# Optimization experiments

Hardware: AMD Instinct MI355X
Metric: run time of the kernel (lower is better)

Reference implementation:

```python
import jax, jax.numpy as jnp
import numpy as np

B, NQ, NK = 4, 2048, 2048
DQ = DK = DV = 256
H = 8
HD = DV // H
EPS = 1e-5


def _ln(x, g, b):
    m = jnp.mean(x, axis=-1, keepdims=True)
    v = jnp.mean(jnp.square(x - m), axis=-1, keepdims=True)
    return (x - m) * jax.lax.rsqrt(v + EPS) * g + b


def setup_inputs() -> dict:
    key = jax.random.key(0)
    ks = jax.random.split(key, 12)
    s = 0.02
    return {
        "Q": jax.random.normal(ks[0], (B, NQ, DQ), jnp.float32),
        "K": jax.random.normal(ks[1], (B, NK, DK), jnp.float32),
        "Wq": jax.random.normal(ks[2], (DV, DQ), jnp.float32) * s,
        "bq": jnp.zeros((DV,), jnp.float32),
        "Wk": jax.random.normal(ks[3], (DV, DK), jnp.float32) * s,
        "bk": jnp.zeros((DV,), jnp.float32),
        "Wv": jax.random.normal(ks[4], (DV, DK), jnp.float32) * s,
        "bv": jnp.zeros((DV,), jnp.float32),
        "Wo": jax.random.normal(ks[5], (DV, DV), jnp.float32) * s,
        "bo": jnp.zeros((DV,), jnp.float32),
        "g0": jnp.ones((DV,), jnp.float32),
        "b0": jnp.zeros((DV,), jnp.float32),
        "g1": jnp.ones((DV,), jnp.float32),
        "b1": jnp.zeros((DV,), jnp.float32),
    }


def reference(Q, K, Wq, bq, Wk, bk, Wv, bv, Wo, bo, g0, b0, g1, b1):
    Qp = Q @ Wq.T + bq            # [B,NQ,DV]
    Kp = K @ Wk.T + bk            # [B,NK,DV]
    Vp = K @ Wv.T + bv            # [B,NK,DV]
    # split(head_dim, dim=2) + cat(dim=0) == reshape heads from contiguous channel chunks
    qh = Qp.reshape(B, NQ, H, HD)
    kh = Kp.reshape(B, NK, H, HD)
    vh = Vp.reshape(B, NK, H, HD)
    scores = jnp.einsum("bqhd,bkhd->bhqk", qh, kh) / jnp.sqrt(jnp.float32(HD))
    attn = jax.nn.softmax(scores, axis=-1)          # [B,H,NQ,NK]
    o = jnp.einsum("bhqk,bkhd->bqhd", attn, vh).reshape(B, NQ, DV)
    o = _ln(o, g0, b0)
    out = o + jax.nn.relu(o @ Wo.T + bo)
    out = _ln(out, g1, b1)
    return out
```

## Files before the change

### kernel.cpp

```cpp
#include <hip/hip_runtime.h>
#include <hip/hip_bf16.h>
#include <math.h>

#define DV 256
#define NH 8
#define NB 4
#define NQ 2048
#define NKK 2048

typedef __attribute__((ext_vector_type(8))) short s8v;
typedef __attribute__((ext_vector_type(16))) float fx16;

typedef const __attribute__((address_space(1))) char g1c;
typedef __attribute__((address_space(3))) char l3c;

__device__ __forceinline__ void gl_lds16(const void* g, void* l) {
    __builtin_amdgcn_global_load_lds((g1c*)g, (l3c*)l, 16, 0, 0);
}
__device__ __forceinline__ unsigned cvtpk_bf16(float lo, float hi) {
    unsigned r;
    asm("v_cvt_pk_bf16_f32 %0, %1, %2" : "=v"(r) : "v"(lo), "v"(hi));
    return r;
}
__device__ __forceinline__ ushort f2bf(float x) {
    unsigned u = __builtin_bit_cast(unsigned, x);
    return (ushort)((u + 0x7fffu + ((u >> 16) & 1u)) >> 16);
}
__device__ __forceinline__ float bf2f(ushort h) {
    return __builtin_bit_cast(float, (unsigned)h << 16);
}

__global__ __launch_bounds__(256) void prep_k(
    const float* __restrict__ Q, const float* __restrict__ K,
    const float* __restrict__ Wq, const float* __restrict__ Wk,
    const float* __restrict__ Wv, const float* __restrict__ Wo,
    ushort* __restrict__ Qc, ushort* __restrict__ Kc, ushort* __restrict__ Wf)
{
    const int i = blockIdx.x * 256 + threadIdx.x;
    const float* src;
    ushort* dst;
    if (i < 262144) {
        src = Q + (size_t)i * 8;  dst = Qc + (size_t)i * 8;
    } else if (i < 524288) {
        src = K + (size_t)(i - 262144) * 8;  dst = Kc + (size_t)(i - 262144) * 8;
    } else {
        const int j = i - 524288;
        const int w = j >> 13, c = j & 8191;
        const int bn = c >> 11, s = (c >> 8) & 7, cc = c & 255;
        const int colblk = cc >> 7, ks = (cc >> 6) & 1, g5 = (cc >> 5) & 1, l31 = cc & 31;
        const int col = bn * 64 + colblk * 32 + l31;
        const int k = s * 32 + ks * 16 + g5 * 8;
        const float* Wsrc = (w == 0) ? Wq : (w == 1) ? Wk : (w == 2) ? Wv : Wo;
        src = Wsrc + (size_t)col * 256 + k;
        dst = Wf + (size_t)j * 8;
    }
    float4 a = *(const float4*)src;
    float4 b = *(const float4*)(src + 4);
    uint4 pk;
    pk.x = cvtpk_bf16(a.x, a.y); pk.y = cvtpk_bf16(a.z, a.w);
    pk.z = cvtpk_bf16(b.x, b.y); pk.w = cvtpk_bf16(b.z, b.w);
    *(uint4*)dst = pk;
}

#define GEMM_MFMA_BODY(A_, WF_)                                                         \
    __shared__ __align__(16) char lds[2][12288];                                        \
    const int t = threadIdx.x, lane = t & 63, wv = t >> 6;                              \
    const int l31 = lane & 31, g5 = lane >> 5;                                          \
    const int bm = blockIdx.x, bn = blockIdx.y;                                         \
    const ushort* asrc0 = A_ + (size_t)(bm * 128 + (t >> 7) * 32 + (t & 31)) * 256      \
                             + ((t >> 6) & 1) * 16 + ((t >> 5) & 1) * 8;                \
    const ushort* asrc1 = asrc0 + 64 * 256;                                             \
    const ushort* wsrc  = WF_ + (size_t)(bn * 8) * 2048 + t * 8;                        \
    gl_lds16(asrc0, &lds[0][wv * 1024]);                                                \
    gl_lds16(asrc1, &lds[0][4096 + wv * 1024]);                                         \
    gl_lds16(wsrc,  &lds[0][8192 + wv * 1024]);                                         \
    __syncthreads();                                                                    \
    fx16 acc0 = {}, acc1 = {};                                                          \
    for (int s = 0; s < 8; ++s) {                                                       \
        const int buf = s & 1;                                                          \
        if (s + 1 < 8) {                                                                \
            gl_lds16(asrc0 + (s + 1) * 32, &lds[buf ^ 1][wv * 1024]);                   \
            gl_lds16(asrc1 + (s + 1) * 32, &lds[buf ^ 1][4096 + wv * 1024]);            \
            gl_lds16(wsrc + (s + 1) * 2048, &lds[buf ^ 1][8192 + wv * 1024]);           \
        }                                                                               \
        const char* Al = lds[buf];                                                      \
        const char* Wl = lds[buf] + 8192;                                               \
        s8v a0  = *(const s8v*)(Al + (wv * 2 + 0) * 1024 + lane * 16);                  \
        s8v a1  = *(const s8v*)(Al + (wv * 2 + 1) * 1024 + lane * 16);                  \
        s8v b00 = *(const s8v*)(Wl + 0 * 1024 + lane * 16);                             \
        s8v b01 = *(const s8v*)(Wl + 1 * 1024 + lane * 16);                             \
        s8v b10 = *(const s8v*)(Wl + 2 * 1024 + lane * 16);                             \
        s8v b11 = *(const s8v*)(Wl + 3 * 1024 + lane * 16);                             \
        __builtin_amdgcn_s_setprio(1);                                                  \
        acc0 = __builtin_amdgcn_mfma_f32_32x32x16_bf16(a0, b00, acc0, 0, 0, 0);         \
        acc0 = __builtin_amdgcn_mfma_f32_32x32x16_bf16(a1, b01, acc0, 0, 0, 0);         \
        acc1 = __builtin_amdgcn_mfma_f32_32x32x16_bf16(a0, b10, acc1, 0, 0, 0);         \
        acc1 = __builtin_amdgcn_mfma_f32_32x32x16_bf16(a1, b11, acc1, 0, 0, 0);         \
        __builtin_amdgcn_s_setprio(0);                                                  \
        __syncthreads();                                                                \
    }                                                                                   \
    const int row_b = bm * 128 + wv * 32;

__global__ __launch_bounds__(256) void gemm_qkv_k(
    const ushort* __restrict__ Qc, const ushort* __restrict__ Kc,
    const ushort* __restrict__ Wf,
    const float* __restrict__ bq, const float* __restrict__ bk, const float* __restrict__ bv,
    ushort* __restrict__ Qb, ushort* __restrict__ Kb, ushort* __restrict__ Vt)
{
    const int z = blockIdx.z;
    const ushort* A  = (z == 0) ? Qc : Kc;
    const ushort* WF = Wf + (size_t)z * 65536;
    const float* bias = (z == 0) ? bq : (z == 1) ? bk : bv;
    GEMM_MFMA_BODY(A, WF)
    const float CE = 0.17677669529663687f * 1.4426950408889634f;
    const float bs0 = bias[bn * 64 + l31];
    const float bs1 = bias[bn * 64 + 32 + l31];
    if (z == 0) {
#pragma unroll
        for (int r = 0; r < 16; ++r) {
            const int row_g = row_b + (r & 3) + 8 * (r >> 2) + 4 * g5;
            Qb[(size_t)row_g * 256 + bn * 64 + l31]      = f2bf((acc0[r] + bs0) * CE);
            Qb[(size_t)row_g * 256 + bn * 64 + 32 + l31] = f2bf((acc1[r] + bs1) * CE);
        }
    } else if (z == 1) {
#pragma unroll
        for (int r = 0; r < 16; ++r) {
            const int row_g = row_b + (r & 3) + 8 * (r >> 2) + 4 * g5;
            Kb[(size_t)row_g * 256 + bn * 64 + l31]      = f2bf(acc0[r] + bs0);
            Kb[(size_t)row_g * 256 + bn * 64 + 32 + l31] = f2bf(acc1[r] + bs1);
        }
    } else {
#pragma unroll
        for (int r = 0; r < 16; ++r) {
            const int row_g = row_b + (r & 3) + 8 * (r >> 2) + 4 * g5;
            const int bb = row_g >> 11, n = row_g & 2047;
            Vt[((size_t)(bb * 8 + bn * 2 + 0) * 32 + l31) * 2048 + n] = f2bf(acc0[r] + bs0);
            Vt[((size_t)(bb * 8 + bn * 2 + 1) * 32 + l31) * 2048 + n] = f2bf(acc1[r] + bs1);
        }
    }
}

__global__ __launch_bounds__(256) void flash_mfma_k(
    const ushort* __restrict__ Qb, const ushort* __restrict__ Kb,
    const ushort* __restrict__ Vt, ushort* __restrict__ Osb, float* __restrict__ L)
{
    __shared__ __align__(16) char lds[2][8192];
    const int t = threadIdx.x;
    const int lane = t & 63, wv = t >> 6;
    const int l31 = lane & 31, g5 = lane >> 5;
    const int qt = blockIdx.x, h = blockIdx.y;
    const int b = blockIdx.z >> 2, sp = blockIdx.z & 3;

    s8v qf0, qf1;
    {
        const ushort* qp = Qb + (((size_t)b * NQ + qt * 128 + wv * 32 + l31) << 8) + h * 32 + g5 * 8;
        qf0 = *(const s8v*)(qp);
        qf1 = *(const s8v*)(qp + 16);
    }
    s8v ones;
#pragma unroll
    for (int j = 0; j < 8; ++j) ones[j] = (short)0x3F80;

    const ushort* ksrc = Kb + (((size_t)b * NKK + sp * 512 + ((t >> 7) * 32 + (t & 31))) << 8)
                            + h * 32 + ((t >> 6) & 1) * 16 + ((t >> 5) & 1) * 8;
    const ushort* vsrc = Vt + (((size_t)(b * NH + h) * 32 + (t & 31)) << 11) + sp * 512
                            + (t >> 6) * 16 + ((t >> 5) & 1) * 8;

    fx16 O0 = {}, lsum = {};

    gl_lds16(ksrc, &lds[0][wv * 1024]);
    gl_lds16(vsrc, &lds[0][4096 + wv * 1024]);
    __syncthreads();

    for (int kt = 0; kt < 8; ++kt) {
        const int buf = kt & 1;
        if (kt + 1 < 8) {
            gl_lds16(ksrc + (size_t)(kt + 1) * 64 * DV, &lds[buf ^ 1][wv * 1024]);
            gl_lds16(vsrc + (kt + 1) * 64, &lds[buf ^ 1][4096 + wv * 1024]);
        }
        const char* Kl = lds[buf];
        const char* Vl = lds[buf] + 4096;
        s8v kf00 = *(const s8v*)(Kl + 0 * 1024 + lane * 16);
        s8v kf01 = *(const s8v*)(Kl + 1 * 1024 + lane * 16);
        s8v kf10 = *(const s8v*)(Kl + 2 * 1024 + lane * 16);
        s8v kf11 = *(const s8v*)(Kl + 3 * 1024 + lane * 16);
        s8v vfa[4];
        vfa[0] = *(const s8v*)(Vl + 0 * 1024 + lane * 16);
        vfa[1] = *(const s8v*)(Vl + 1 * 1024 + lane * 16);
        vfa[2] = *(const s8v*)(Vl + 2 * 1024 + lane * 16);
        vfa[3] = *(const s8v*)(Vl + 3 * 1024 + lane * 16);

        fx16 z = {};
        __builtin_amdgcn_s_setprio(1);
        fx16 Sa = __builtin_amdgcn_mfma_f32_32x32x16_bf16(kf00, qf0, z, 0, 0, 0);
        Sa = __builtin_amdgcn_mfma_f32_32x32x16_bf16(kf01, qf1, Sa, 0, 0, 0);
        fx16 Sb = __builtin_amdgcn_mfma_f32_32x32x16_bf16(kf10, qf0, z, 0, 0, 0);
        Sb = __builtin_amdgcn_mfma_f32_32x32x16_bf16(kf11, qf1, Sb, 0, 0, 0);
        __builtin_amdgcn_s_setprio(0);

        float p[32];
#pragma unroll
        for (int i = 0; i < 16; ++i) {
            p[i]      = __builtin_amdgcn_exp2f(Sa[i]);
            p[16 + i] = __builtin_amdgcn_exp2f(Sb[i]);
        }

        __builtin_amdgcn_s_setprio(1);
#pragma unroll
        for (int kt2 = 0; kt2 < 4; ++kt2) {
            const int pb = 8 * kt2;
            auto ra = __builtin_amdgcn_permlane32_swap(
                cvtpk_bf16(p[pb + 0], p[pb + 1]), cvtpk_bf16(p[pb + 4], p[pb + 5]), false, false);
            auto rb = __builtin_amdgcn_permlane32_swap(
                cvtpk_bf16(p[pb + 2], p[pb + 3]), cvtpk_bf16(p[pb + 6], p[pb + 7]), false, false);
            union { unsigned u[4]; s8v v; } pf;
            pf.u[0] = ra[0]; pf.u[1] = rb[0]; pf.u[2] = ra[1]; pf.u[3] = rb[1];
            O0   = __builtin_amdgcn_mfma_f32_32x32x16_bf16(vfa[kt2], pf.v, O0, 0, 0, 0);
            lsum = __builtin_amdgcn_mfma_f32_32x32x16_bf16(ones,    pf.v, lsum, 0, 0, 0);
        }
        __builtin_amdgcn_s_setprio(0);
        __syncthreads();
    }

    {
        const int qrow = qt * 128 + wv * 32 + l31;
        ushort* dst0 = Osb + (size_t)sp * (8192 * 256)
                     + (((size_t)b * NQ + qrow) << 8) + h * 32 + g5 * 4;
#pragma unroll
        for (int rr = 0; rr < 4; ++rr) {
            uint2 w;
            w.x = cvtpk_bf16(O0[4 * rr + 0], O0[4 * rr + 1]);
            w.y = cvtpk_bf16(O0[4 * rr + 2], O0[4 * rr + 3]);
            *(uint2*)(dst0 + 8 * rr) = w;
        }
        if (g5 == 0)
            L[(((size_t)sp * NB + b) * NH + h) * NQ + qrow] = lsum[0];
    }
}

__global__ __launch_bounds__(256) void comb_ln_k(
    const ushort* __restrict__ Osb, const float* __restrict__ L,
    const float* __restrict__ g, const float* __restrict__ bb,
    ushort* __restrict__ Yb)
{
    const int t = threadIdx.x, lane = t & 63, w = t >> 6;
    const int row = blockIdx.x * 4 + w;
    const int b = row >> 11, q = row & 2047;
    const int h = lane >> 3;
    const size_t lbase = (((size_t)b * NH + h) * NQ + q);
    const size_t LS = (size_t)NB * NH * NQ;
    const float lt = (L[lbase] + L[LS + lbase]) + (L[2 * LS + lbase] + L[3 * LS + lbase]);
    const float inv = 1.f / lt;
    const size_t SZS = (size_t)8192 * 256;
    const size_t off = (size_t)row * 256 + lane * 4;
    const ushort4 x0 = *(const ushort4*)(Osb + off);
    const ushort4 x1 = *(const ushort4*)(Osb + SZS + off);
    const ushort4 x2 = *(const ushort4*)(Osb + 2 * SZS + off);
    const ushort4 x3 = *(const ushort4*)(Osb + 3 * SZS + off);
    float4 x;
    x.x = ((bf2f(x0.x) + bf2f(x1.x)) + (bf2f(x2.x) + bf2f(x3.x))) * inv;
    x.y = ((bf2f(x0.y) + bf2f(x1.y)) + (bf2f(x2.y) + bf2f(x3.y))) * inv;
    x.z = ((bf2f(x0.z) + bf2f(x1.z)) + (bf2f(x2.z) + bf2f(x3.z))) * inv;
    x.w = ((bf2f(x0.w) + bf2f(x1.w)) + (bf2f(x2.w) + bf2f(x3.w))) * inv;
    float s  = (x.x + x.y) + (x.z + x.w);
    float sq = fmaf(x.x, x.x, fmaf(x.y, x.y, fmaf(x.z, x.z, x.w * x.w)));
    for (int off2 = 32; off2; off2 >>= 1) {
        s  += __shfl_xor(s, off2);
        sq += __shfl_xor(sq, off2);
    }
    const float mean = s * (1.f / 256.f);
    const float var  = sq * (1.f / 256.f) - mean * mean;
    const float ri   = rsqrtf(var + 1e-5f);
    const float4 gv = *(const float4*)(g + lane * 4);
    const float4 bv = *(const float4*)(bb + lane * 4);
    uint2 p;
    p.x = cvtpk_bf16((x.x - mean) * ri * gv.x + bv.x, (x.y - mean) * ri * gv.y + bv.y);
    p.y = cvtpk_bf16((x.z - mean) * ri * gv.z + bv.z, (x.w - mean) * ri * gv.w + bv.w);
    *(uint2*)(Yb + (size_t)row * 256 + lane * 4) = p;
}

__global__ __launch_bounds__(256) void gemm_ln_k(
    const ushort* __restrict__ Ain, const ushort* __restrict__ Wfo,
    const float* __restrict__ bo, const float* __restrict__ g1,
    const float* __restrict__ b1, float* __restrict__ out)
{
    __shared__ __align__(16) char alds[32768];
    __shared__ __align__(16) char wlds[2][16384];
    __shared__ float red[4][64][2];
    __shared__ float par[64][2];
    const int t = threadIdx.x, lane = t & 63, wv = t >> 6;
    const int l31 = lane & 31, g5 = lane >> 5;
    const int row0 = blockIdx.x * 64;

#pragma unroll
    for (int it = 0; it < 8; ++it) {
        const int id = it * 256 + t;
        const int s = id >> 8, rem = id & 255, kc = rem >> 6, row = rem & 63;
        gl_lds16(Ain + (size_t)(row0 + row) * 256 + s * 32 + (kc >> 1) * 16 + (kc & 1) * 8,
                 &alds[id * 16]);
    }
#pragma unroll
    for (int it = 0; it < 4; ++it) {
        const int id = it * 256 + t;
        gl_lds16(Wfo + ((size_t)(id >> 8) * 2048 + (id & 255)) * 8, &wlds[0][id * 16]);
    }
    __syncthreads();

    fx16 acc[2][2] = {};
    for (int s = 0; s < 8; ++s) {
        const int buf = s & 1;
        if (s + 1 < 8) {
#pragma unroll
            for (int it = 0; it < 4; ++it) {
                const int id = it * 256 + t;
                gl_lds16(Wfo + ((size_t)(id >> 8) * 2048 + (s + 1) * 256 + (id & 255)) * 8,
                         &wlds[buf ^ 1][id * 16]);
            }
        }
        s8v a[2][2], bf[2][2];
#pragma unroll
        for (int rb = 0; rb < 2; ++rb)
#pragma unroll
            for (int ks = 0; ks < 2; ++ks)
                a[rb][ks] = *(const s8v*)(alds + ((s * 4 + ks * 2 + g5) * 64 + rb * 32 + l31) * 16);
#pragma unroll
        for (int ks = 0; ks < 2; ++ks)
#pragma unroll
            for (int ch = 0; ch < 2; ++ch)
                bf[ks][ch] = *(const s8v*)(wlds[buf] + (wv * 256 + ch * 128 + ks * 64 + g5 * 32 + l31) * 16);
        __builtin_amdgcn_s_setprio(1);
#pragma unroll
        for (int rb = 0; rb < 2; ++rb)
#pragma unroll
            for (int ch = 0; ch < 2; ++ch) {
                acc[rb][ch] = __builtin_amdgcn_mfma_f32_32x32x16_bf16(a[rb][0], bf[0][ch], acc[rb][ch], 0, 0, 0);
                acc[rb][ch] = __builtin_amdgcn_mfma_f32_32x32x16_bf16(a[rb][1], bf[1][ch], acc[rb][ch], 0, 0, 0);
            }
        __builtin_amdgcn_s_setprio(0);
        __syncthreads();
    }

    const int cg0 = wv * 64 + l31, cg1 = cg0 + 32;
    const float bo0 = bo[cg0], bo1 = bo[cg1];
    const int s0 = cg0 >> 5, kk0 = cg0 & 31;
    const int s1 = cg1 >> 5, kk1 = cg1 & 31;
    const int coff0 = (s0 * 4 + ((kk0 >> 4) << 1) + ((kk0 >> 3) & 1)) * 64;
    const int coff1 = (s1 * 4 + ((kk1 >> 4) << 1) + ((kk1 >> 3) & 1)) * 64;
    float x[2][2][16];
#pragma unroll
    for (int rb = 0; rb < 2; ++rb) {
#pragma unroll
        for (int r = 0; r < 16; ++r) {
            const int row = rb * 32 + (r & 3) + 8 * (r >> 2) + 4 * g5;
            const ushort h0v = *(const ushort*)(alds + ((coff0 + row) << 4) + (kk0 & 7) * 2);
            const ushort h1v = *(const ushort*)(alds + ((coff1 + row) << 4) + (kk1 & 7) * 2);
            const float x0 = bf2f(h0v) + fmaxf(acc[rb][0][r] + bo0, 0.f);
            const float x1 = bf2f(h1v) + fmaxf(acc[rb][1][r] + bo1, 0.f);
            x[rb][0][r] = x0; x[rb][1][r] = x1;
            float sv = x0 + x1;
            float sq = fmaf(x0, x0, x1 * x1);
#pragma unroll
            for (int off = 1; off < 32; off <<= 1) {
                sv += __shfl_xor(sv, off);
                sq += __shfl_xor(sq, off);
            }
            if (l31 == 0) { red[wv][row][0] = sv; red[wv][row][1] = sq; }
        }
    }
    __syncthreads();
    if (t < 64) {
        const float sv = (red[0][t][0] + red[1][t][0]) + (red[2][t][0] + red[3][t][0]);
        const float sq = (red[0][t][1] + red[1][t][1]) + (red[2][t][1] + red[3][t][1]);
        const float mean = sv * (1.f / 256.f);
        const float var  = sq * (1.f / 256.f) - mean * mean;
        par[t][0] = mean;
        par[t][1] = rsqrtf(var + 1e-5f);
    }
    __syncthreads();
    const float g1a = g1[cg0], g1b = g1[cg1];
    const float b1a = b1[cg0], b1b = b1[cg1];
#pragma unroll
    for (int rb = 0; rb < 2; ++rb) {
#pragma unroll
        for (int r = 0; r < 16; ++r) {
            const int row = rb * 32 + (r & 3) + 8 * (r >> 2) + 4 * g5;
            const float mean = par[row][0], ri = par[row][1];
            out[(size_t)(row0 + row) * 256 + cg0] = (x[rb][0][r] - mean) * ri * g1a + b1a;
            out[(size_t)(row0 + row) * 256 + cg1] = (x[rb][1][r] - mean) * ri * g1b + b1b;
        }
    }
}

extern "C" void kernel_launch(void* const* d_in, const int* in_sizes, int n_in,
                              void* d_out, int out_size, void* d_ws, size_t ws_size,
                              hipStream_t stream) {
    const float* Q  = (const float*)d_in[0];
    const float* K  = (const float*)d_in[1];
    const float* Wq = (const float*)d_in[2];
    const float* bq = (const float*)d_in[3];
    const float* Wk = (const float*)d_in[4];
    const float* bk = (const float*)d_in[5];
    const float* Wv = (const float*)d_in[6];
    const float* bv = (const float*)d_in[7];
    const float* Wo = (const float*)d_in[8];
    const float* bo = (const float*)d_in[9];
    const float* g0 = (const float*)d_in[10];
    const float* b0 = (const float*)d_in[11];
    const float* g1 = (const float*)d_in[12];
    const float* b1 = (const float*)d_in[13];
    float* out = (float*)d_out;

    char* wsb = (char*)d_ws;
    const size_t MB = 1u << 20;
    ushort* Qc  = (ushort*)(wsb + 14 * MB);
    ushort* Kc  = (ushort*)(wsb + 18 * MB);
    ushort* Wf  = (ushort*)(wsb + 13 * MB);
    ushort* Qb  = (ushort*)(wsb + 1 * MB);
    ushort* Kb  = (ushort*)(wsb + 5 * MB);
    ushort* Vt  = (ushort*)(wsb + 9 * MB);
    ushort* Osb = (ushort*)(wsb + 14 * MB);
    float*  L   = (float*)(wsb + 30 * MB);
    ushort* h0b = (ushort*)(wsb + 9 * MB);

    prep_k<<<2176, 256, 0, stream>>>(Q, K, Wq, Wk, Wv, Wo, Qc, Kc, Wf);
    gemm_qkv_k<<<dim3(64, 4, 3), 256, 0, stream>>>(Qc, Kc, Wf, bq, bk, bv, Qb, Kb, Vt);
    flash_mfma_k<<<dim3(16, 8, 16), 256, 0, stream>>>(Qb, Kb, Vt, Osb, L);
    comb_ln_k<<<2048, 256, 0, stream>>>(Osb, L, g0, b0, h0b);
    gemm_ln_k<<<128, 256, 0, stream>>>(h0b, Wf + 3 * 65536, bo, g1, b1, out);
}
```

Baseline: 77.21 us.

## Fuse fp32-to-bf16 input conversion into QKV GEMM and halve flash KV splits

Drops the separate pass that converts Q and K to bf16. The QKV GEMM now streams the fp32 inputs straight into LDS and converts them in registers before the MFMAs, so prep only converts the weights. Separately, the flash-attention split-K factor goes from 4 to 2: each block walks 1024 keys over 16 tiles, and the combine kernel reads two partials instead of four. This removes a full read and write of the activations and halves the partial-output traffic, at the cost of twice the A-tile bytes per GEMM stage and half as many flash blocks (1024 instead of 2048).

```diff
diff --git a/kernel.cpp b/kernel.cpp
--- a/kernel.cpp
+++ b/kernel.cpp
@@ -30,88 +30,93 @@
     return __builtin_bit_cast(float, (unsigned)h << 16);
 }
 
-__global__ __launch_bounds__(256) void prep_k(
-    const float* __restrict__ Q, const float* __restrict__ K,
+__global__ __launch_bounds__(256) void prep_w_k(
     const float* __restrict__ Wq, const float* __restrict__ Wk,
     const float* __restrict__ Wv, const float* __restrict__ Wo,
-    ushort* __restrict__ Qc, ushort* __restrict__ Kc, ushort* __restrict__ Wf)
+    ushort* __restrict__ Wf)
 {
-    const int i = blockIdx.x * 256 + threadIdx.x;
-    const float* src;
-    ushort* dst;
-    if (i < 262144) {
-        src = Q + (size_t)i * 8;  dst = Qc + (size_t)i * 8;
-    } else if (i < 524288) {
-        src = K + (size_t)(i - 262144) * 8;  dst = Kc + (size_t)(i - 262144) * 8;
-    } else {
-        const int j = i - 524288;
-        const int w = j >> 13, c = j & 8191;
-        const int bn = c >> 11, s = (c >> 8) & 7, cc = c & 255;
-        const int colblk = cc >> 7, ks = (cc >> 6) & 1, g5 = (cc >> 5) & 1, l31 = cc & 31;
-        const int col = bn * 64 + colblk * 32 + l31;
-        const int k = s * 32 + ks * 16 + g5 * 8;
-        const float* Wsrc = (w == 0) ? Wq : (w == 1) ? Wk : (w == 2) ? Wv : Wo;
-        src = Wsrc + (size_t)col * 256 + k;
-        dst = Wf + (size_t)j * 8;
-    }
+    const int j = blockIdx.x * 256 + threadIdx.x;
+    const int w = j >> 13, c = j & 8191;
+    const int bn = c >> 11, s = (c >> 8) & 7, cc = c & 255;
+    const int colblk = cc >> 7, ks = (cc >> 6) & 1, g5w = (cc >> 5) & 1, l31w = cc & 31;
+    const int col = bn * 64 + colblk * 32 + l31w;
+    const int k = s * 32 + ks * 16 + g5w * 8;
+    const float* Wsrc = (w == 0) ? Wq : (w == 1) ? Wk : (w == 2) ? Wv : Wo;
+    const float* src = Wsrc + (size_t)col * 256 + k;
     float4 a = *(const float4*)src;
     float4 b = *(const float4*)(src + 4);
     uint4 pk;
     pk.x = cvtpk_bf16(a.x, a.y); pk.y = cvtpk_bf16(a.z, a.w);
     pk.z = cvtpk_bf16(b.x, b.y); pk.w = cvtpk_bf16(b.z, b.w);
-    *(uint4*)dst = pk;
-}
-
-#define GEMM_MFMA_BODY(A_, WF_)                                                         \
-    __shared__ __align__(16) char lds[2][12288];                                        \
-    const int t = threadIdx.x, lane = t & 63, wv = t >> 6;                              \
-    const int l31 = lane & 31, g5 = lane >> 5;                                          \
-    const int bm = blockIdx.x, bn = blockIdx.y;                                         \
-    const ushort* asrc0 = A_ + (size_t)(bm * 128 + (t >> 7) * 32 + (t & 31)) * 256      \
-                             + ((t >> 6) & 1) * 16 + ((t >> 5) & 1) * 8;                \
-    const ushort* asrc1 = asrc0 + 64 * 256;                                             \
-    const ushort* wsrc  = WF_ + (size_t)(bn * 8) * 2048 + t * 8;                        \
-    gl_lds16(asrc0, &lds[0][wv * 1024]);                                                \
-    gl_lds16(asrc1, &lds[0][4096 + wv * 1024]);                                         \
-    gl_lds16(wsrc,  &lds[0][8192 + wv * 1024]);                                         \
-    __syncthreads();                                                                    \
-    fx16 acc0 = {}, acc1 = {};                                                          \
-    for (int s = 0; s < 8; ++s) {                                                       \
-        const int buf = s & 1;                                                          \
-        if (s + 1 < 8) {                                                                \
-            gl_lds16(asrc0 + (s + 1) * 32, &lds[buf ^ 1][wv * 1024]);                   \
-            gl_lds16(asrc1 + (s + 1) * 32, &lds[buf ^ 1][4096 + wv * 1024]);            \
-            gl_lds16(wsrc + (s + 1) * 2048, &lds[buf ^ 1][8192 + wv * 1024]);           \
-        }                                                                               \
-        const char* Al = lds[buf];                                                      \
-        const char* Wl = lds[buf] + 8192;                                               \
-        s8v a0  = *(const s8v*)(Al + (wv * 2 + 0) * 1024 + lane * 16);                  \
-        s8v a1  = *(const s8v*)(Al + (wv * 2 + 1) * 1024 + lane * 16);                  \
-        s8v b00 = *(const s8v*)(Wl + 0 * 1024 + lane * 16);                             \
-        s8v b01 = *(const s8v*)(Wl + 1 * 1024 + lane * 16);                             \
-        s8v b10 = *(const s8v*)(Wl + 2 * 1024 + lane * 16);                             \
-        s8v b11 = *(const s8v*)(Wl + 3 * 1024 + lane * 16);                             \
-        __builtin_amdgcn_s_setprio(1);                                                  \
-        acc0 = __builtin_amdgcn_mfma_f32_32x32x16_bf16(a0, b00, acc0, 0, 0, 0);         \
-        acc0 = __builtin_amdgcn_mfma_f32_32x32x16_bf16(a1, b01, acc0, 0, 0, 0);         \
-        acc1 = __builtin_amdgcn_mfma_f32_32x32x16_bf16(a0, b10, acc1, 0, 0, 0);         \
-        acc1 = __builtin_amdgcn_mfma_f32_32x32x16_bf16(a1, b11, acc1, 0, 0, 0);         \
-        __builtin_amdgcn_s_setprio(0);                                                  \
-        __syncthreads();                                                                \
-    }                                                                                   \
-    const int row_b = bm * 128 + wv * 32;
+    *(uint4*)(Wf + (size_t)j * 8) = pk;
+}
 
 __global__ __launch_bounds__(256) void gemm_qkv_k(
-    const ushort* __restrict__ Qc, const ushort* __restrict__ Kc,
+    const float* __restrict__ Qf, const float* __restrict__ Kf,
     const ushort* __restrict__ Wf,
     const float* __restrict__ bq, const float* __restrict__ bk, const float* __restrict__ bv,
     ushort* __restrict__ Qb, ushort* __restrict__ Kb, ushort* __restrict__ Vt)
 {
+    __shared__ __align__(16) char lds[2][20480];
+    const int t = threadIdx.x, lane = t & 63, wv = t >> 6;
+    const int l31 = lane & 31, g5 = lane >> 5;
+    const int bm = blockIdx.x, bn = blockIdx.y;
     const int z = blockIdx.z;
-    const ushort* A  = (z == 0) ? Qc : Kc;
+    const float* Af = (z == 0) ? Qf : Kf;
     const ushort* WF = Wf + (size_t)z * 65536;
     const float* bias = (z == 0) ? bq : (z == 1) ? bk : bv;
-    GEMM_MFMA_BODY(A, WF)
+
+    int arow[4], aoff[4];
+#pragma unroll
+    for (int k = 0; k < 4; ++k) {
+        const int q = k * 256 + t, c = q >> 1, p = q & 1;
+        arow[k] = bm * 128 + (c >> 7) * 32 + (c & 31);
+        aoff[k] = ((c >> 6) & 1) * 16 + ((c >> 5) & 1) * 8 + p * 4;
+    }
+    const ushort* wsrc = WF + (size_t)(bn * 8) * 2048 + t * 8;
+
+#pragma unroll
+    for (int k = 0; k < 4; ++k)
+        gl_lds16(Af + (size_t)arow[k] * 256 + aoff[k],
+                 &lds[0][k * 4096 + wv * 1024 + lane * 16]);
+    gl_lds16(wsrc, &lds[0][16384 + wv * 1024 + lane * 16]);
+    __syncthreads();
+
+    fx16 acc0 = {}, acc1 = {};
+    for (int s = 0; s < 8; ++s) {
+        const int buf = s & 1;
+        if (s + 1 < 8) {
+#pragma unroll
+            for (int k = 0; k < 4; ++k)
+                gl_lds16(Af + (size_t)arow[k] * 256 + (s + 1) * 32 + aoff[k],
+                         &lds[buf ^ 1][k * 4096 + wv * 1024 + lane * 16]);
+            gl_lds16(wsrc + (s + 1) * 2048, &lds[buf ^ 1][16384 + wv * 1024 + lane * 16]);
+        }
+        const char* Al = lds[buf];
+        const char* Wl = lds[buf] + 16384;
+        float4 fa0 = *(const float4*)(Al + (wv * 2 + 0) * 2048 + lane * 32);
+        float4 fb0 = *(const float4*)(Al + (wv * 2 + 0) * 2048 + lane * 32 + 16);
+        float4 fa1 = *(const float4*)(Al + (wv * 2 + 1) * 2048 + lane * 32);
+        float4 fb1 = *(const float4*)(Al + (wv * 2 + 1) * 2048 + lane * 32 + 16);
+        union { unsigned u[4]; s8v v; } A0, A1;
+        A0.u[0] = cvtpk_bf16(fa0.x, fa0.y); A0.u[1] = cvtpk_bf16(fa0.z, fa0.w);
+        A0.u[2] = cvtpk_bf16(fb0.x, fb0.y); A0.u[3] = cvtpk_bf16(fb0.z, fb0.w);
+        A1.u[0] = cvtpk_bf16(fa1.x, fa1.y); A1.u[1] = cvtpk_bf16(fa1.z, fa1.w);
+        A1.u[2] = cvtpk_bf16(fb1.x, fb1.y); A1.u[3] = cvtpk_bf16(fb1.z, fb1.w);
+        s8v b00 = *(const s8v*)(Wl + 0 * 1024 + lane * 16);
+        s8v b01 = *(const s8v*)(Wl + 1 * 1024 + lane * 16);
+        s8v b10 = *(const s8v*)(Wl + 2 * 1024 + lane * 16);
+        s8v b11 = *(const s8v*)(Wl + 3 * 1024 + lane * 16);
+        __builtin_amdgcn_s_setprio(1);
+        acc0 = __builtin_amdgcn_mfma_f32_32x32x16_bf16(A0.v, b00, acc0, 0, 0, 0);
+        acc0 = __builtin_amdgcn_mfma_f32_32x32x16_bf16(A1.v, b01, acc0, 0, 0, 0);
+        acc1 = __builtin_amdgcn_mfma_f32_32x32x16_bf16(A0.v, b10, acc1, 0, 0, 0);
+        acc1 = __builtin_amdgcn_mfma_f32_32x32x16_bf16(A1.v, b11, acc1, 0, 0, 0);
+        __builtin_amdgcn_s_setprio(0);
+        __syncthreads();
+    }
+
+    const int row_b = bm * 128 + wv * 32;
     const float CE = 0.17677669529663687f * 1.4426950408889634f;
     const float bs0 = bias[bn * 64 + l31];
     const float bs1 = bias[bn * 64 + 32 + l31];
@@ -149,7 +154,7 @@
     const int lane = t & 63, wv = t >> 6;
     const int l31 = lane & 31, g5 = lane >> 5;
     const int qt = blockIdx.x, h = blockIdx.y;
-    const int b = blockIdx.z >> 2, sp = blockIdx.z & 3;
+    const int b = blockIdx.z >> 1, sp = blockIdx.z & 1;
 
     s8v qf0, qf1;
     {
@@ -161,9 +166,9 @@
 #pragma unroll
     for (int j = 0; j < 8; ++j) ones[j] = (short)0x3F80;
 
-    const ushort* ksrc = Kb + (((size_t)b * NKK + sp * 512 + ((t >> 7) * 32 + (t & 31))) << 8)
+    const ushort* ksrc = Kb + (((size_t)b * NKK + sp * 1024 + ((t >> 7) * 32 + (t & 31))) << 8)
                             + h * 32 + ((t >> 6) & 1) * 16 + ((t >> 5) & 1) * 8;
-    const ushort* vsrc = Vt + (((size_t)(b * NH + h) * 32 + (t & 31)) << 11) + sp * 512
+    const ushort* vsrc = Vt + (((size_t)(b * NH + h) * 32 + (t & 31)) << 11) + sp * 1024
                             + (t >> 6) * 16 + ((t >> 5) & 1) * 8;
 
     fx16 O0 = {}, lsum = {};
@@ -172,9 +177,9 @@
     gl_lds16(vsrc, &lds[0][4096 + wv * 1024]);
     __syncthreads();
 
-    for (int kt = 0; kt < 8; ++kt) {
+    for (int kt = 0; kt < 16; ++kt) {
         const int buf = kt & 1;
-        if (kt + 1 < 8) {
+        if (kt + 1 < 16) {
             gl_lds16(ksrc + (size_t)(kt + 1) * 64 * DV, &lds[buf ^ 1][wv * 1024]);
             gl_lds16(vsrc + (kt + 1) * 64, &lds[buf ^ 1][4096 + wv * 1024]);
         }
@@ -249,19 +254,16 @@
     const int h = lane >> 3;
     const size_t lbase = (((size_t)b * NH + h) * NQ + q);
     const size_t LS = (size_t)NB * NH * NQ;
-    const float lt = (L[lbase] + L[LS + lbase]) + (L[2 * LS + lbase] + L[3 * LS + lbase]);
-    const float inv = 1.f / lt;
+    const float inv = 1.f / (L[lbase] + L[LS + lbase]);
     const size_t SZS = (size_t)8192 * 256;
     const size_t off = (size_t)row * 256 + lane * 4;
     const ushort4 x0 = *(const ushort4*)(Osb + off);
     const ushort4 x1 = *(const ushort4*)(Osb + SZS + off);
-    const ushort4 x2 = *(const ushort4*)(Osb + 2 * SZS + off);
-    const ushort4 x3 = *(const ushort4*)(Osb + 3 * SZS + off);
     float4 x;
-    x.x = ((bf2f(x0.x) + bf2f(x1.x)) + (bf2f(x2.x) + bf2f(x3.x))) * inv;
-    x.y = ((bf2f(x0.y) + bf2f(x1.y)) + (bf2f(x2.y) + bf2f(x3.y))) * inv;
-    x.z = ((bf2f(x0.z) + bf2f(x1.z)) + (bf2f(x2.z) + bf2f(x3.z))) * inv;
-    x.w = ((bf2f(x0.w) + bf2f(x1.w)) + (bf2f(x2.w) + bf2f(x3.w))) * inv;
+    x.x = (bf2f(x0.x) + bf2f(x1.x)) * inv;
+    x.y = (bf2f(x0.y) + bf2f(x1.y)) * inv;
+    x.z = (bf2f(x0.z) + bf2f(x1.z)) * inv;
+    x.w = (bf2f(x0.w) + bf2f(x1.w)) * inv;
     float s  = (x.x + x.y) + (x.z + x.w);
     float sq = fmaf(x.x, x.x, fmaf(x.y, x.y, fmaf(x.z, x.z, x.w * x.w)));
     for (int off2 = 32; off2; off2 >>= 1) {
@@ -412,19 +414,17 @@
 
     char* wsb = (char*)d_ws;
     const size_t MB = 1u << 20;
-    ushort* Qc  = (ushort*)(wsb + 14 * MB);
-    ushort* Kc  = (ushort*)(wsb + 18 * MB);
-    ushort* Wf  = (ushort*)(wsb + 13 * MB);
-    ushort* Qb  = (ushort*)(wsb + 1 * MB);
-    ushort* Kb  = (ushort*)(wsb + 5 * MB);
-    ushort* Vt  = (ushort*)(wsb + 9 * MB);
-    ushort* Osb = (ushort*)(wsb + 14 * MB);
-    float*  L   = (float*)(wsb + 30 * MB);
-    ushort* h0b = (ushort*)(wsb + 9 * MB);
-
-    prep_k<<<2176, 256, 0, stream>>>(Q, K, Wq, Wk, Wv, Wo, Qc, Kc, Wf);
-    gemm_qkv_k<<<dim3(64, 4, 3), 256, 0, stream>>>(Qc, Kc, Wf, bq, bk, bv, Qb, Kb, Vt);
-    flash_mfma_k<<<dim3(16, 8, 16), 256, 0, stream>>>(Qb, Kb, Vt, Osb, L);
+    ushort* Wf  = (ushort*)(wsb + 12 * MB);
+    ushort* Qb  = (ushort*)(wsb + 0 * MB);
+    ushort* Kb  = (ushort*)(wsb + 4 * MB);
+    ushort* Vt  = (ushort*)(wsb + 8 * MB);
+    ushort* Osb = (ushort*)(wsb + 13 * MB);
+    float*  L   = (float*)(wsb + 21 * MB);
+    ushort* h0b = (ushort*)(wsb + 8 * MB);
+
+    prep_w_k<<<128, 256, 0, stream>>>(Wq, Wk, Wv, Wo, Wf);
+    gemm_qkv_k<<<dim3(64, 4, 3), 256, 0, stream>>>(Q, K, Wf, bq, bk, bv, Qb, Kb, Vt);
+    flash_mfma_k<<<dim3(16, 8, 8), 256, 0, stream>>>(Qb, Kb, Vt, Osb, L);
     comb_ln_k<<<2048, 256, 0, stream>>>(Osb, L, g0, b0, h0b);
     gemm_ln_k<<<128, 256, 0, stream>>>(h0b, Wf + 3 * 65536, bo, g1, b1, out);
 }
```

Result: no change. 78.44 us (+1.6%).
